# Kernel tuning notes

Measured on AMD Instinct MI355X. Metric: run time of the kernel, lower is better.

Reference implementation:

```python
import jax, jax.numpy as jnp
import numpy as np

A, B = 8192, 8192
E1, E2, C = 1024, 1024, 1024
M = min(E1, E2)


def setup_inputs() -> dict:
    key = jax.random.key(0)
    ks = jax.random.split(key, 9)
    s = lambda fan_in: 1.0 / np.sqrt(fan_in)
    return {
        "seq1_ae": jax.random.normal(ks[0], (A, E1), jnp.float32),
        "seq2_be": jax.random.normal(ks[1], (B, E2), jnp.float32),
        "context_c": jax.random.normal(ks[2], (C,), jnp.float32),
        "W_ctx1": jax.random.uniform(ks[3], (M, C), jnp.float32, -s(C), s(C)),
        "W_ctx2": jax.random.uniform(ks[4], (M, C), jnp.float32, -s(C), s(C)),
        "W1": jax.random.uniform(ks[5], (M, E1), jnp.float32, -s(E1), s(E1)),
        "b1": jax.random.uniform(ks[6], (M,), jnp.float32, -s(E1), s(E1)),
        "W2": jax.random.uniform(ks[7], (M, E2), jnp.float32, -s(E2), s(E2)),
        "b2": jax.random.uniform(ks[8], (M,), jnp.float32, -s(E2), s(E2)),
    }


def reference(seq1_ae, seq2_be, context_c, W_ctx1, W_ctx2, W1, b1, W2, b2):
    ctx1_m = W_ctx1 @ context_c                      # [m]
    ctx2_m = W_ctx2 @ context_c                      # [m]
    p1_am = jax.nn.elu(seq1_ae @ W1.T + b1 + ctx1_m) # [a, m]
    p2_bm = jax.nn.elu(seq2_be @ W2.T + b2 + ctx2_m) # [b, m]
    matrix_ab = p1_am @ p2_bm.T                      # [a, b]
    logits_a = matrix_ab.sum(1)                      # [a]
    logits_b = matrix_ab.sum(0)                      # [b]
    att1 = seq1_ae.T @ jax.nn.softmax(logits_a)      # [e1]
    att2 = seq2_be.T @ jax.nn.softmax(logits_b)      # [e2]
    return (att1, att2)
```

## Files before the change

### kernel.cpp

```cpp
#include <hip/hip_runtime.h>
#include <hip/hip_bf16.h>


#define A_ROWS 8192
#define EDIM   1024
#define MDIM   1024

typedef __attribute__((ext_vector_type(8))) short bf16x8;
typedef __attribute__((ext_vector_type(4))) int i32x4;

#define OFF_BIAS1   0ull
#define OFF_BIAS2   4096ull
#define OFF_S1      8192ull
#define OFF_S2      12288ull
#define OFF_LOGA    16384ull
#define OFF_P1      81920ull
#define OFF_P2      (OFF_P1 + 16777216ull)
#define OFF_SEQ1B   (OFF_P2 + 16777216ull)
#define OFF_SEQ2B   (OFF_SEQ1B + 16777216ull)
#define OFF_W1B     (OFF_SEQ2B + 16777216ull)
#define OFF_W2B     (OFF_W1B + 2097152ull)

#define SA_INV 21.166666f
#define SW_INV 4064.0f
#define SP_INV 25.4f
#define DQ_P   (5.0f / 127.0f)
#define DQ_A   (6.0f / 127.0f)

__device__ __forceinline__ unsigned pack4(float4 f, float s) {
  int q0 = __float2int_rn(f.x * s); q0 = q0 > 127 ? 127 : (q0 < -127 ? -127 : q0);
  int q1 = __float2int_rn(f.y * s); q1 = q1 > 127 ? 127 : (q1 < -127 ? -127 : q1);
  int q2 = __float2int_rn(f.z * s); q2 = q2 > 127 ? 127 : (q2 < -127 ? -127 : q2);
  int q3 = __float2int_rn(f.w * s); q3 = q3 > 127 ? 127 : (q3 < -127 ? -127 : q3);
  return (q0 & 255) | ((q1 & 255) << 8) | ((q2 & 255) << 16) | ((q3 & 255) << 24);
}

#define GLOAD16(src, dst) __builtin_amdgcn_global_load_lds( \
    (const __attribute__((address_space(1))) void*)(src),   \
    (__attribute__((address_space(3))) void*)(dst), 16, 0, 0)

__global__ __launch_bounds__(256) void prep_k(
    const float* __restrict__ s1, const float* __restrict__ s2,
    const float* __restrict__ w1, const float* __restrict__ w2,
    uint2* __restrict__ s1o, uint2* __restrict__ s2o,
    uint2* __restrict__ w1o, uint2* __restrict__ w2o,
    const float* __restrict__ Wc1, const float* __restrict__ Wc2,
    const float* __restrict__ ctx, const float* __restrict__ b1,
    const float* __restrict__ b2, float* __restrict__ bias1,
    float* __restrict__ bias2, float* __restrict__ S1, float* __restrict__ S2,
    float* __restrict__ outz) {
  int z = blockIdx.z;
  if (z < 4) {
    const float* in = z == 0 ? s1 : z == 1 ? s2 : z == 2 ? w1 : w2;
    uint2* out = z == 0 ? s1o : z == 1 ? s2o : z == 2 ? w1o : w2o;
    float sc = z < 2 ? SA_INV : SW_INV;
    int n8 = z < 2 ? (A_ROWS * EDIM / 8) : (MDIM * EDIM / 8);
    int stride = gridDim.x * blockDim.x;
    for (int i = blockIdx.x * blockDim.x + threadIdx.x; i < n8; i += stride) {
      float4 fa = reinterpret_cast<const float4*>(in)[2 * i];
      float4 fb = reinterpret_cast<const float4*>(in)[2 * i + 1];
      out[i] = make_uint2(pack4(fa, sc), pack4(fb, sc));
    }
  } else {
    if (blockIdx.x == 0) {
      float4 zv = make_float4(0.f, 0.f, 0.f, 0.f);
      ((float4*)outz)[threadIdx.x] = zv;
      ((float4*)outz)[threadIdx.x + 256] = zv;
    }
    if (blockIdx.x >= 512) return;
    int zz = blockIdx.x >= 256;
    int bx = blockIdx.x & 255;
    const float* W = zz ? Wc2 : Wc1;
    const float* b = zz ? b2 : b1;
    float* bias = zz ? bias2 : bias1;
    float* S = zz ? S2 : S1;
    int wave = threadIdx.x >> 6, lane = threadIdx.x & 63;
    int m = bx * 4 + wave;
    const float4* wr = reinterpret_cast<const float4*>(W + (size_t)m * EDIM);
    const float4* cv = reinterpret_cast<const float4*>(ctx);
    float acc = 0.f;
#pragma unroll
    for (int ch = 0; ch < 4; ++ch) {
      float4 a = wr[ch * 64 + lane], d = cv[ch * 64 + lane];
      acc += a.x * d.x + a.y * d.y + a.z * d.z + a.w * d.w;
    }
    for (int o = 32; o; o >>= 1) acc += __shfl_down(acc, o);
    if (lane == 0) { bias[m] = acc + b[m]; S[m] = 0.f; }
  }
}

__global__ __launch_bounds__(512) void gemm8(
    const char* __restrict__ A1, const char* __restrict__ A2,
    const char* __restrict__ B1, const char* __restrict__ B2,
    const float* __restrict__ bias1, const float* __restrict__ bias2,
    char* __restrict__ P1, char* __restrict__ P2,
    float* __restrict__ S1, float* __restrict__ S2) {
  const int z = blockIdx.z;
  const char* __restrict__ Ab = z ? A2 : A1;
  const char* __restrict__ Bb = z ? B2 : B1;
  const float* __restrict__ bias = z ? bias2 : bias1;
  char* __restrict__ P = z ? P2 : P1;
  float* __restrict__ S = z ? S2 : S1;

  __shared__ __align__(16) char ldsb[131072];

  const int tid = threadIdx.x;
  const int lane = tid & 63;
  const int wave = tid >> 6;
  const int wm = wave >> 2, wn = wave & 3;
  const int r = lane & 15, kq = lane >> 4;
  const int brow = blockIdx.x * 256, bcol = blockIdx.y * 256;
  const int wrow = wm * 128, wcol = wn * 64;

  const int xm = (r & 7) << 4;
  const int aB0 = wm * 16384 + r * 128 + ((kq * 16) ^ xm);
  const int aB1 = wm * 16384 + r * 128 + ((64 + kq * 16) ^ xm);
  const int bRow = (wn & 1) * 64 + r;
  const int bB0 = 65536 + (wn >> 1) * 16384 + bRow * 128 + ((kq * 16) ^ xm);
  const int bB1 = 65536 + (wn >> 1) * 16384 + bRow * 128 + ((64 + kq * 16) ^ xm);

  const int srow = tid >> 3;
  const int scb = ((tid & 7) * 16) ^ ((srow & 7) << 4);
  const char* aSrc = Ab + (size_t)(brow + srow) * 1024 + scb;
  const char* bSrc = Bb + (size_t)(bcol + srow) * 1024 + scb;

#define STG_A(buf, h, kt) do { \
    const char* s_ = aSrc + (h) * 131072 + (kt) * 128; \
    char* d_ = ldsb + (buf) * 32768 + (h) * 16384 + tid * 16; \
    GLOAD16(s_, d_); GLOAD16(s_ + 65536, d_ + 8192); } while (0)
#define STG_B(buf, h, kt) do { \
    const char* s_ = bSrc + (h) * 131072 + (kt) * 128; \
    char* d_ = ldsb + 65536 + (buf) * 32768 + (h) * 16384 + tid * 16; \
    GLOAD16(s_, d_); GLOAD16(s_ + 65536, d_ + 8192); } while (0)
#define RD_A0(buf, mf) (*(const i32x4*)(ldsb + aB0 + (buf) * 32768 + (mf) * 2048))
#define RD_A1(buf, mf) (*(const i32x4*)(ldsb + aB1 + (buf) * 32768 + (mf) * 2048))
#define RD_B0(buf, nf) (*(const i32x4*)(ldsb + bB0 + (buf) * 32768 + (nf) * 2048))
#define RD_B1(buf, nf) (*(const i32x4*)(ldsb + bB1 + (buf) * 32768 + (nf) * 2048))
#define VMW4 asm volatile("s_waitcnt vmcnt(4)" ::: "memory")
#define VMW0 asm volatile("s_waitcnt vmcnt(0)" ::: "memory")
#define BAR __builtin_amdgcn_s_barrier()
#define MF(a, b, c) __builtin_amdgcn_mfma_i32_16x16x64_i8((a), (b), (c), 0, 0, 0)
#define LDA(buf, mf0) do { a0k0 = RD_A0(buf, mf0); a0k1 = RD_A1(buf, mf0); \
    a1k0 = RD_A0(buf, (mf0) + 1); a1k1 = RD_A1(buf, (mf0) + 1); } while (0)
#define LDB(buf) do { \
    b0k0 = RD_B0(buf, 0); b0k1 = RD_B1(buf, 0); b1k0 = RD_B0(buf, 1); b1k1 = RD_B1(buf, 1); \
    b2k0 = RD_B0(buf, 2); b2k1 = RD_B1(buf, 2); b3k0 = RD_B0(buf, 3); b3k1 = RD_B1(buf, 3); } while (0)
#define QUAD(q) do { __builtin_amdgcn_s_setprio(1); \
    acc[q][0] = MF(a0k0, b0k0, acc[q][0]); acc[q][0] = MF(a0k1, b0k1, acc[q][0]); \
    acc[q][1] = MF(a0k0, b1k0, acc[q][1]); acc[q][1] = MF(a0k1, b1k1, acc[q][1]); \
    acc[q][2] = MF(a0k0, b2k0, acc[q][2]); acc[q][2] = MF(a0k1, b2k1, acc[q][2]); \
    acc[q][3] = MF(a0k0, b3k0, acc[q][3]); acc[q][3] = MF(a0k1, b3k1, acc[q][3]); \
    acc[(q)+1][0] = MF(a1k0, b0k0, acc[(q)+1][0]); acc[(q)+1][0] = MF(a1k1, b0k1, acc[(q)+1][0]); \
    acc[(q)+1][1] = MF(a1k0, b1k0, acc[(q)+1][1]); acc[(q)+1][1] = MF(a1k1, b1k1, acc[(q)+1][1]); \
    acc[(q)+1][2] = MF(a1k0, b2k0, acc[(q)+1][2]); acc[(q)+1][2] = MF(a1k1, b2k1, acc[(q)+1][2]); \
    acc[(q)+1][3] = MF(a1k0, b3k0, acc[(q)+1][3]); acc[(q)+1][3] = MF(a1k1, b3k1, acc[(q)+1][3]); \
    __builtin_amdgcn_s_setprio(0); } while (0)

  i32x4 acc[8][4] = {};
  i32x4 a0k0, a0k1, a1k0, a1k1;
  i32x4 b0k0, b0k1, b1k0, b1k1, b2k0, b2k1, b3k0, b3k1;

  STG_B(0, 0, 0); STG_B(0, 1, 0); STG_A(0, 0, 0); STG_A(0, 1, 0);
  STG_B(1, 0, 1); STG_B(1, 1, 1);

  for (int it = 0; it < 3; ++it) {
    const int k1 = 2 * it + 1;
    const int k2 = 2 * it + 2;
    const int k3 = 2 * it + 3;
    VMW4; BAR;
    LDB(0); LDA(0, 0); STG_A(1, 0, k1); QUAD(0);
    BAR; LDA(0, 2); STG_A(1, 1, k1); QUAD(2);
    BAR; LDA(0, 4); STG_B(0, 0, k2); QUAD(4);
    BAR; LDA(0, 6); STG_B(0, 1, k2); QUAD(6);
    VMW4; BAR;
    LDB(1); LDA(1, 0); STG_A(0, 0, k2); QUAD(0);
    BAR; LDA(1, 2); STG_A(0, 1, k2); QUAD(2);
    BAR; LDA(1, 4); STG_B(1, 0, k3); QUAD(4);
    BAR; LDA(1, 6); STG_B(1, 1, k3); QUAD(6);
  }
  VMW4; BAR;
  LDB(0); LDA(0, 0); STG_A(1, 0, 7); QUAD(0);
  BAR; LDA(0, 2); STG_A(1, 1, 7); QUAD(2);
  BAR; LDA(0, 4); QUAD(4);
  BAR; LDA(0, 6); QUAD(6);
  VMW0; BAR;
  LDB(1); LDA(1, 0); QUAD(0);
  BAR; LDA(1, 2); QUAD(2);
  BAR; LDA(1, 4); QUAD(4);
  BAR; LDA(1, 6); QUAD(6);
  BAR;

  const float DQ = (6.0f / 127.0f) * (0.03125f / 127.0f);
  char* pl = ldsb;
  float bv[4], cs[4] = {0.f, 0.f, 0.f, 0.f};
#pragma unroll
  for (int nf = 0; nf < 4; ++nf) bv[nf] = bias[bcol + wcol + nf * 16 + r];
#pragma unroll
  for (int mf = 0; mf < 8; ++mf)
#pragma unroll
    for (int nf = 0; nf < 4; ++nf)
#pragma unroll
      for (int j = 0; j < 4; ++j) {
        float v = (float)acc[mf][nf][j] * DQ + bv[nf];
        v = v > 0.f ? v : (__expf(v) - 1.f);
        cs[nf] += v;
        int q = __float2int_rn(v * SP_INV);
        q = q > 127 ? 127 : (q < -127 ? -127 : q);
        int row = wrow + mf * 16 + kq * 4 + j;
        pl[row * 256 + wcol + nf * 16 + r] = (char)q;
      }
#pragma unroll
  for (int nf = 0; nf < 4; ++nf) {
    cs[nf] += __shfl_xor(cs[nf], 16);
    cs[nf] += __shfl_xor(cs[nf], 32);
    if (kq == 0) atomicAdd(&S[bcol + wcol + nf * 16 + r], cs[nf]);
  }
  __syncthreads();
#pragma unroll
  for (int i = 0; i < 8; ++i) {
    int c = i * 512 + tid;
    int row = c >> 4, coff = (c & 15) * 16;
    *(uint4*)(P + (size_t)(brow + row) * MDIM + bcol + coff) =
        *(const uint4*)(pl + row * 256 + coff);
  }
#undef STG_A
#undef STG_B
#undef RD_A0
#undef RD_A1
#undef RD_B0
#undef RD_B1
#undef VMW4
#undef VMW0
#undef BAR
#undef MF
#undef LDA
#undef LDB
#undef QUAD
}

__global__ __launch_bounds__(256) void gemv_logits_k(
    const char* __restrict__ P1, const char* __restrict__ P2,
    const float* __restrict__ S1, const float* __restrict__ S2,
    float* __restrict__ L) {
  int z = blockIdx.z;
  const char* P = z ? P2 : P1;
  const float* s = z ? S1 : S2;
  float* Lz = L + (size_t)z * 8192;
  int wave = threadIdx.x >> 6, lane = threadIdx.x & 63;
  int row = blockIdx.x * 4 + wave;
  uint4 w = *(const uint4*)(P + (size_t)row * MDIM + lane * 16);
  const float4* sv = reinterpret_cast<const float4*>(s + lane * 16);
  float4 s0 = sv[0], s1v = sv[1], s2v = sv[2], s3v = sv[3];
  float acc =
      (float)(char)(w.x) * s0.x + (float)(char)(w.x >> 8) * s0.y +
      (float)(char)(w.x >> 16) * s0.z + (float)(char)(w.x >> 24) * s0.w +
      (float)(char)(w.y) * s1v.x + (float)(char)(w.y >> 8) * s1v.y +
      (float)(char)(w.y >> 16) * s1v.z + (float)(char)(w.y >> 24) * s1v.w +
      (float)(char)(w.z) * s2v.x + (float)(char)(w.z >> 8) * s2v.y +
      (float)(char)(w.z >> 16) * s2v.z + (float)(char)(w.z >> 24) * s2v.w +
      (float)(char)(w.w) * s3v.x + (float)(char)(w.w >> 8) * s3v.y +
      (float)(char)(w.w >> 16) * s3v.z + (float)(char)(w.w >> 24) * s3v.w;
  for (int o = 32; o; o >>= 1) acc += __shfl_down(acc, o);
  if (lane == 0) Lz[row] = acc * DQ_P;
}

__global__ __launch_bounds__(256) void att_sm_k(const char* __restrict__ s1b,
    const char* __restrict__ s2b, const float* __restrict__ logits,
    float* __restrict__ out) {
  int z = blockIdx.z;
  const char* seq = z ? s2b : s1b;
  const float* L = logits + (size_t)z * 8192;
  float* o = out + (size_t)z * EDIM;
  __shared__ float red[256];
  __shared__ float wsm[128];
  int tid = threadIdx.x;

  float lv[32];
  float m = -3.4e38f;
#pragma unroll
  for (int k = 0; k < 32; ++k) { lv[k] = L[tid + k * 256]; m = fmaxf(m, lv[k]); }
  red[tid] = m; __syncthreads();
  for (int s = 128; s; s >>= 1) {
    if (tid < s) red[tid] = fmaxf(red[tid], red[tid + s]);
    __syncthreads();
  }
  m = red[0]; __syncthreads();
  float sum = 0.f;
#pragma unroll
  for (int k = 0; k < 32; ++k) sum += __expf(lv[k] - m);
  red[tid] = sum; __syncthreads();
  for (int s = 128; s; s >>= 1) {
    if (tid < s) red[tid] += red[tid + s];
    __syncthreads();
  }
  float inv = 1.f / red[0];

  int a0 = blockIdx.y * 128;
  if (tid < 128) wsm[tid] = __expf(L[a0 + tid] - m) * inv;
  __syncthreads();

  float c0 = 0.f, c1 = 0.f, c2 = 0.f, c3 = 0.f;
  const char* p = seq + (size_t)a0 * EDIM + tid * 4;
#pragma unroll 4
  for (int j = 0; j < 128; ++j, p += EDIM) {
    float wa = wsm[j];
    unsigned v = *reinterpret_cast<const unsigned*>(p);
    c0 += wa * (float)(char)(v);
    c1 += wa * (float)(char)(v >> 8);
    c2 += wa * (float)(char)(v >> 16);
    c3 += wa * (float)(char)(v >> 24);
  }
  atomicAdd(&o[tid * 4 + 0], c0 * DQ_A);
  atomicAdd(&o[tid * 4 + 1], c1 * DQ_A);
  atomicAdd(&o[tid * 4 + 2], c2 * DQ_A);
  atomicAdd(&o[tid * 4 + 3], c3 * DQ_A);
}

extern "C" void kernel_launch(void* const* d_in, const int* in_sizes, int n_in,
                              void* d_out, int out_size, void* d_ws, size_t ws_size,
                              hipStream_t stream) {
  const float* seq1 = (const float*)d_in[0];
  const float* seq2 = (const float*)d_in[1];
  const float* ctx  = (const float*)d_in[2];
  const float* Wc1  = (const float*)d_in[3];
  const float* Wc2  = (const float*)d_in[4];
  const float* W1   = (const float*)d_in[5];
  const float* b1   = (const float*)d_in[6];
  const float* W2   = (const float*)d_in[7];
  const float* b2   = (const float*)d_in[8];
  float* out = (float*)d_out;
  char* ws = (char*)d_ws;

  float* bias1 = (float*)(ws + OFF_BIAS1);
  float* bias2 = (float*)(ws + OFF_BIAS2);
  float* s1    = (float*)(ws + OFF_S1);
  float* s2    = (float*)(ws + OFF_S2);
  float* loga  = (float*)(ws + OFF_LOGA);
  char* p1     = (char*)(ws + OFF_P1);
  char* p2     = (char*)(ws + OFF_P2);
  char* seq1b  = (char*)(ws + OFF_SEQ1B);
  char* seq2b  = (char*)(ws + OFF_SEQ2B);
  char* w1b    = (char*)(ws + OFF_W1B);
  char* w2b    = (char*)(ws + OFF_W2B);

  prep_k<<<dim3(512, 1, 5), 256, 0, stream>>>(
      seq1, seq2, W1, W2, (uint2*)seq1b, (uint2*)seq2b, (uint2*)w1b, (uint2*)w2b,
      Wc1, Wc2, ctx, b1, b2, bias1, bias2, s1, s2, out);

  gemm8<<<dim3(A_ROWS / 256, MDIM / 256, 2), 512, 0, stream>>>(
      seq1b, seq2b, w1b, w2b, bias1, bias2, p1, p2, s1, s2);

  gemv_logits_k<<<dim3(2048, 1, 2), 256, 0, stream>>>(p1, p2, s1, s2, loga);

  att_sm_k<<<dim3(1, 64, 2), 256, 0, stream>>>(seq1b, seq2b, loga, out);
}
```

Before: 67.69 us.

## Load GEMM B operand directly from global into registers, halve LDS, split attention finer

The int8 GEMM stops staging the weight (B) tile through shared memory. Each wave now loads its B fragments straight from global memory into registers, double-buffered across k-steps, which halves LDS use to 64KB and allows two blocks per CU via launch bounds. The barriers between quads are dropped in favour of one barrier per tile. The attention kernel is split into twice as many blocks of 64 rows to raise parallelism. The cost is more global/L2 traffic for B, since each wave fetches its own copy, and higher register pressure from the sixteen B registers.

```diff
diff --git a/kernel.cpp b/kernel.cpp
--- a/kernel.cpp
+++ b/kernel.cpp
@@ -6,7 +6,6 @@
 #define EDIM   1024
 #define MDIM   1024
 
-typedef __attribute__((ext_vector_type(8))) short bf16x8;
 typedef __attribute__((ext_vector_type(4))) int i32x4;
 
 #define OFF_BIAS1   0ull
@@ -89,7 +88,7 @@
   }
 }
 
-__global__ __launch_bounds__(512) void gemm8(
+__global__ __launch_bounds__(512, 2) void gemm8(
     const char* __restrict__ A1, const char* __restrict__ A2,
     const char* __restrict__ B1, const char* __restrict__ B2,
     const float* __restrict__ bias1, const float* __restrict__ bias2,
@@ -102,7 +101,7 @@
   char* __restrict__ P = z ? P2 : P1;
   float* __restrict__ S = z ? S2 : S1;
 
-  __shared__ __align__(16) char ldsb[131072];
+  __shared__ __align__(16) char ldsb[65536];
 
   const int tid = threadIdx.x;
   const int lane = tid & 63;
@@ -115,79 +114,74 @@
   const int xm = (r & 7) << 4;
   const int aB0 = wm * 16384 + r * 128 + ((kq * 16) ^ xm);
   const int aB1 = wm * 16384 + r * 128 + ((64 + kq * 16) ^ xm);
-  const int bRow = (wn & 1) * 64 + r;
-  const int bB0 = 65536 + (wn >> 1) * 16384 + bRow * 128 + ((kq * 16) ^ xm);
-  const int bB1 = 65536 + (wn >> 1) * 16384 + bRow * 128 + ((64 + kq * 16) ^ xm);
 
   const int srow = tid >> 3;
   const int scb = ((tid & 7) * 16) ^ ((srow & 7) << 4);
   const char* aSrc = Ab + (size_t)(brow + srow) * 1024 + scb;
-  const char* bSrc = Bb + (size_t)(bcol + srow) * 1024 + scb;
+
+  const char* bPtr = Bb + (size_t)(bcol + wn * 64 + r) * 1024 + kq * 16;
 
 #define STG_A(buf, h, kt) do { \
     const char* s_ = aSrc + (h) * 131072 + (kt) * 128; \
     char* d_ = ldsb + (buf) * 32768 + (h) * 16384 + tid * 16; \
     GLOAD16(s_, d_); GLOAD16(s_ + 65536, d_ + 8192); } while (0)
-#define STG_B(buf, h, kt) do { \
-    const char* s_ = bSrc + (h) * 131072 + (kt) * 128; \
-    char* d_ = ldsb + 65536 + (buf) * 32768 + (h) * 16384 + tid * 16; \
-    GLOAD16(s_, d_); GLOAD16(s_ + 65536, d_ + 8192); } while (0)
 #define RD_A0(buf, mf) (*(const i32x4*)(ldsb + aB0 + (buf) * 32768 + (mf) * 2048))
 #define RD_A1(buf, mf) (*(const i32x4*)(ldsb + aB1 + (buf) * 32768 + (mf) * 2048))
-#define RD_B0(buf, nf) (*(const i32x4*)(ldsb + bB0 + (buf) * 32768 + (nf) * 2048))
-#define RD_B1(buf, nf) (*(const i32x4*)(ldsb + bB1 + (buf) * 32768 + (nf) * 2048))
 #define VMW4 asm volatile("s_waitcnt vmcnt(4)" ::: "memory")
 #define VMW0 asm volatile("s_waitcnt vmcnt(0)" ::: "memory")
 #define BAR __builtin_amdgcn_s_barrier()
 #define MF(a, b, c) __builtin_amdgcn_mfma_i32_16x16x64_i8((a), (b), (c), 0, 0, 0)
 #define LDA(buf, mf0) do { a0k0 = RD_A0(buf, mf0); a0k1 = RD_A1(buf, mf0); \
     a1k0 = RD_A0(buf, (mf0) + 1); a1k1 = RD_A1(buf, (mf0) + 1); } while (0)
-#define LDB(buf) do { \
-    b0k0 = RD_B0(buf, 0); b0k1 = RD_B1(buf, 0); b1k0 = RD_B0(buf, 1); b1k1 = RD_B1(buf, 1); \
-    b2k0 = RD_B0(buf, 2); b2k1 = RD_B1(buf, 2); b3k0 = RD_B0(buf, 3); b3k1 = RD_B1(buf, 3); } while (0)
-#define QUAD(q) do { __builtin_amdgcn_s_setprio(1); \
-    acc[q][0] = MF(a0k0, b0k0, acc[q][0]); acc[q][0] = MF(a0k1, b0k1, acc[q][0]); \
-    acc[q][1] = MF(a0k0, b1k0, acc[q][1]); acc[q][1] = MF(a0k1, b1k1, acc[q][1]); \
-    acc[q][2] = MF(a0k0, b2k0, acc[q][2]); acc[q][2] = MF(a0k1, b2k1, acc[q][2]); \
-    acc[q][3] = MF(a0k0, b3k0, acc[q][3]); acc[q][3] = MF(a0k1, b3k1, acc[q][3]); \
-    acc[(q)+1][0] = MF(a1k0, b0k0, acc[(q)+1][0]); acc[(q)+1][0] = MF(a1k1, b0k1, acc[(q)+1][0]); \
-    acc[(q)+1][1] = MF(a1k0, b1k0, acc[(q)+1][1]); acc[(q)+1][1] = MF(a1k1, b1k1, acc[(q)+1][1]); \
-    acc[(q)+1][2] = MF(a1k0, b2k0, acc[(q)+1][2]); acc[(q)+1][2] = MF(a1k1, b2k1, acc[(q)+1][2]); \
-    acc[(q)+1][3] = MF(a1k0, b3k0, acc[(q)+1][3]); acc[(q)+1][3] = MF(a1k1, b3k1, acc[(q)+1][3]); \
+#define LOADB(S, kt) do { \
+    S##0 = *(const i32x4*)(bPtr + (size_t)(kt) * 128); \
+    S##1 = *(const i32x4*)(bPtr + (size_t)(kt) * 128 + 64); \
+    S##2 = *(const i32x4*)(bPtr + (size_t)(kt) * 128 + 16384); \
+    S##3 = *(const i32x4*)(bPtr + (size_t)(kt) * 128 + 16384 + 64); \
+    S##4 = *(const i32x4*)(bPtr + (size_t)(kt) * 128 + 32768); \
+    S##5 = *(const i32x4*)(bPtr + (size_t)(kt) * 128 + 32768 + 64); \
+    S##6 = *(const i32x4*)(bPtr + (size_t)(kt) * 128 + 49152); \
+    S##7 = *(const i32x4*)(bPtr + (size_t)(kt) * 128 + 49152 + 64); } while (0)
+#define QUAD(q, S) do { __builtin_amdgcn_s_setprio(1); \
+    acc[q][0] = MF(a0k0, S##0, acc[q][0]); acc[q][0] = MF(a0k1, S##1, acc[q][0]); \
+    acc[q][1] = MF(a0k0, S##2, acc[q][1]); acc[q][1] = MF(a0k1, S##3, acc[q][1]); \
+    acc[q][2] = MF(a0k0, S##4, acc[q][2]); acc[q][2] = MF(a0k1, S##5, acc[q][2]); \
+    acc[q][3] = MF(a0k0, S##6, acc[q][3]); acc[q][3] = MF(a0k1, S##7, acc[q][3]); \
+    acc[(q)+1][0] = MF(a1k0, S##0, acc[(q)+1][0]); acc[(q)+1][0] = MF(a1k1, S##1, acc[(q)+1][0]); \
+    acc[(q)+1][1] = MF(a1k0, S##2, acc[(q)+1][1]); acc[(q)+1][1] = MF(a1k1, S##3, acc[(q)+1][1]); \
+    acc[(q)+1][2] = MF(a1k0, S##4, acc[(q)+1][2]); acc[(q)+1][2] = MF(a1k1, S##5, acc[(q)+1][2]); \
+    acc[(q)+1][3] = MF(a1k0, S##6, acc[(q)+1][3]); acc[(q)+1][3] = MF(a1k1, S##7, acc[(q)+1][3]); \
     __builtin_amdgcn_s_setprio(0); } while (0)
+#define TILE(buf, S) do { \
+    LDA(buf, 0); QUAD(0, S); LDA(buf, 2); QUAD(2, S); \
+    LDA(buf, 4); QUAD(4, S); LDA(buf, 6); QUAD(6, S); } while (0)
 
   i32x4 acc[8][4] = {};
   i32x4 a0k0, a0k1, a1k0, a1k1;
-  i32x4 b0k0, b0k1, b1k0, b1k1, b2k0, b2k1, b3k0, b3k1;
-
-  STG_B(0, 0, 0); STG_B(0, 1, 0); STG_A(0, 0, 0); STG_A(0, 1, 0);
-  STG_B(1, 0, 1); STG_B(1, 1, 1);
+  i32x4 p0, p1, p2, p3, p4, p5, p6, p7;
+  i32x4 q0, q1, q2, q3, q4, q5, q6, q7;
+
+  STG_A(0, 0, 0); STG_A(0, 1, 0); STG_A(1, 0, 1); STG_A(1, 1, 1);
+  LOADB(p, 0);
 
   for (int it = 0; it < 3; ++it) {
-    const int k1 = 2 * it + 1;
-    const int k2 = 2 * it + 2;
-    const int k3 = 2 * it + 3;
     VMW4; BAR;
-    LDB(0); LDA(0, 0); STG_A(1, 0, k1); QUAD(0);
-    BAR; LDA(0, 2); STG_A(1, 1, k1); QUAD(2);
-    BAR; LDA(0, 4); STG_B(0, 0, k2); QUAD(4);
-    BAR; LDA(0, 6); STG_B(0, 1, k2); QUAD(6);
+    LOADB(q, 2 * it + 1);
+    TILE(0, p);
+    BAR;
+    STG_A(0, 0, 2 * it + 2); STG_A(0, 1, 2 * it + 2);
     VMW4; BAR;
-    LDB(1); LDA(1, 0); STG_A(0, 0, k2); QUAD(0);
-    BAR; LDA(1, 2); STG_A(0, 1, k2); QUAD(2);
-    BAR; LDA(1, 4); STG_B(1, 0, k3); QUAD(4);
-    BAR; LDA(1, 6); STG_B(1, 1, k3); QUAD(6);
+    LOADB(p, 2 * it + 2);
+    TILE(1, q);
+    BAR;
+    STG_A(1, 0, 2 * it + 3); STG_A(1, 1, 2 * it + 3);
   }
   VMW4; BAR;
-  LDB(0); LDA(0, 0); STG_A(1, 0, 7); QUAD(0);
-  BAR; LDA(0, 2); STG_A(1, 1, 7); QUAD(2);
-  BAR; LDA(0, 4); QUAD(4);
-  BAR; LDA(0, 6); QUAD(6);
+  LOADB(q, 7);
+  TILE(0, p);
+  BAR;
   VMW0; BAR;
-  LDB(1); LDA(1, 0); QUAD(0);
-  BAR; LDA(1, 2); QUAD(2);
-  BAR; LDA(1, 4); QUAD(4);
-  BAR; LDA(1, 6); QUAD(6);
+  TILE(1, q);
   BAR;
 
   const float DQ = (6.0f / 127.0f) * (0.03125f / 127.0f);
@@ -224,18 +218,16 @@
         *(const uint4*)(pl + row * 256 + coff);
   }
 #undef STG_A
-#undef STG_B
 #undef RD_A0
 #undef RD_A1
-#undef RD_B0
-#undef RD_B1
 #undef VMW4
 #undef VMW0
 #undef BAR
 #undef MF
 #undef LDA
-#undef LDB
+#undef LOADB
 #undef QUAD
+#undef TILE
 }
 
 __global__ __launch_bounds__(256) void gemv_logits_k(
@@ -272,7 +264,7 @@
   const float* L = logits + (size_t)z * 8192;
   float* o = out + (size_t)z * EDIM;
   __shared__ float red[256];
-  __shared__ float wsm[128];
+  __shared__ float wsm[64];
   int tid = threadIdx.x;
 
   float lv[32];
@@ -295,14 +287,14 @@
   }
   float inv = 1.f / red[0];
 
-  int a0 = blockIdx.y * 128;
-  if (tid < 128) wsm[tid] = __expf(L[a0 + tid] - m) * inv;
+  int a0 = blockIdx.y * 64;
+  if (tid < 64) wsm[tid] = __expf(L[a0 + tid] - m) * inv;
   __syncthreads();
 
   float c0 = 0.f, c1 = 0.f, c2 = 0.f, c3 = 0.f;
   const char* p = seq + (size_t)a0 * EDIM + tid * 4;
 #pragma unroll 4
-  for (int j = 0; j < 128; ++j, p += EDIM) {
+  for (int j = 0; j < 64; ++j, p += EDIM) {
     float wa = wsm[j];
     unsigned v = *reinterpret_cast<const unsigned*>(p);
     c0 += wa * (float)(char)(v);
@@ -352,5 +344,5 @@
 
   gemv_logits_k<<<dim3(2048, 1, 2), 256, 0, stream>>>(p1, p2, s1, s2, loga);
 
-  att_sm_k<<<dim3(1, 64, 2), 256, 0, stream>>>(seq1b, seq2b, loga, out);
-}
+  att_sm_k<<<dim3(1, 128, 2), 256, 0, stream>>>(seq1b, seq2b, loga, out);
+}
```

New measurement: 78.90 us. +16.6%, slower.
